# Kernel tuning notes

Hardware: AMD Instinct MI355X
Metric: run time of the kernel (lower is better)

The kernel has to match this reference:

```python
import jax, jax.numpy as jnp
import numpy as np

B = 65536
IN = 64
H = 16
PF = 64


def _linear_params(key, out_dim, in_dim):
    k1, k2 = jax.random.split(key)
    bound = 1.0 / np.sqrt(in_dim)
    W = jax.random.uniform(k1, (out_dim, in_dim), jnp.float32, -bound, bound)
    b = jax.random.uniform(k2, (out_dim,), jnp.float32, -bound, bound)
    return W, b


def setup_inputs() -> dict:
    key = jax.random.key(0)
    ks = jax.random.split(key, 20)
    inp = {}
    for i, name in enumerate(['a', 'v', 'l', 'p_a', 'p_v', 'p_l', 'mean']):
        inp[name] = jax.random.normal(ks[i], (B, IN), jnp.float32)
    inp['Wa'], inp['ba'] = _linear_params(ks[7], H, IN)
    inp['Wv'], inp['bv'] = _linear_params(ks[8], H, IN)
    inp['Wl'], inp['bl'] = _linear_params(ks[9], H, IN)
    inp['Wap'], inp['bap'] = _linear_params(ks[10], H, IN)
    inp['Wvp'], inp['bvp'] = _linear_params(ks[11], H, IN)
    inp['Wlp'], inp['blp'] = _linear_params(ks[12], H, IN)
    inp['Wf1'], inp['bf1'] = _linear_params(ks[13], PF, H ** 3 // 16)
    inp['Wfp1'], inp['bfp1'] = _linear_params(ks[14], PF, H ** 3 // 16)
    inp['Wng'], inp['bng'] = _linear_params(ks[15], 64, 128)
    inp['rm1'] = jnp.zeros((128,), jnp.float32)  # normGate2 running_mean buffers (eval mode)
    inp['rm2'] = jnp.zeros((128,), jnp.float32)
    return inp


def _maxpool2(x):
    # 2x2 stride-2 max pool over the last two dims of [B, Hd, Wd]
    b, hd, wd = x.shape
    return x.reshape(b, hd // 2, 2, wd // 2, 2).max(axis=(2, 4))


def _trimodal_fusion(x_h, y_h, z_h):
    # outer product [B,H,H] -> pool -> [B,H*H//4,1] bmm [B,1,H] -> pool -> flatten
    f = x_h[:, :, None] * y_h[:, None, :]            # [B,16,16]
    f = _maxpool2(f)                                 # [B,8,8]
    f = f.reshape(-1, H * H // 4, 1) * z_h[:, None, :]  # [B,64,16]
    f = _maxpool2(f)                                 # [B,32,8]
    return f.reshape(x_h.shape[0], -1)               # [B,256]


def _norm_gate(x, running_mean):
    # eval-mode normGate2: y = x * sigmoid(|x - running_mean|)
    return x * jax.nn.sigmoid(jnp.abs(x - running_mean))


def reference(a, v, l, p_a, p_v, p_l, mean,
              Wa, ba, Wv, bv, Wl, bl, Wap, bap, Wvp, bvp, Wlp, blp,
              Wf1, bf1, Wfp1, bfp1, Wng, bng, rm1, rm2):
    a_h = jax.nn.sigmoid(a @ Wa.T + ba)
    v_h = jax.nn.sigmoid(v @ Wv.T + bv)
    l_h = jax.nn.sigmoid(l @ Wl.T + bl)
    fusion_1 = jax.nn.leaky_relu(_trimodal_fusion(a_h, v_h, l_h) @ Wf1.T + bf1)

    pa_h = jax.nn.sigmoid(p_a @ Wap.T + bap)
    pv_h = jax.nn.sigmoid(p_v @ Wvp.T + bvp)
    pl_h = jax.nn.sigmoid(p_l @ Wlp.T + blp)
    fusion_2 = jax.nn.leaky_relu(_trimodal_fusion(pa_h, pv_h, pl_h) @ Wfp1.T + bfp1)

    out = _norm_gate(jnp.concatenate([fusion_2, mean], axis=1), rm1)   # [B,128]
    out = out @ Wng.T + bng                                            # [B,64]
    out = _norm_gate(jnp.concatenate([out, fusion_1], axis=1), rm2)    # [B,128]
    return out
```

## Files before the change

kernel.cpp:

```cpp
#include <hip/hip_runtime.h>
#include <hip/hip_bf16.h>


typedef __attribute__((ext_vector_type(8))) short short8;
typedef __attribute__((ext_vector_type(4))) float f32x4;

#define MFMA16(A, B, C) __builtin_amdgcn_mfma_f32_16x16x32_bf16((A), (B), (C), 0, 0, 0)

__device__ __forceinline__ float fast_sigmoid(float x) {
    return __builtin_amdgcn_rcpf(1.0f + __expf(-x));
}
__device__ __forceinline__ float gate(float x, float rm) {
    return x * fast_sigmoid(fabsf(x - rm));
}
__device__ __forceinline__ float lrelu(float x) {
    return x >= 0.0f ? x : 0.01f * x;
}
__device__ __forceinline__ short f2bf(float f) {
    union { float f; unsigned u; } x; x.f = f;
    unsigned r = (x.u + 0x7FFF + ((x.u >> 16) & 1)) >> 16;
    return (short)r;
}
__device__ __forceinline__ short8 pack8(const float* xs) {
    union { short8 s; __hip_bfloat162 h[4]; } u;
    #pragma unroll
    for (int i = 0; i < 4; ++i) {
        float2 t; t.x = xs[2 * i]; t.y = xs[2 * i + 1];
        u.h[i] = __float22bfloat162_rn(t);
    }
    return u.s;
}
__device__ __forceinline__ f32x4 pmax_xor(f32x4 v, int mask) {
    f32x4 r;
    #pragma unroll
    for (int i = 0; i < 4; ++i) r[i] = fmaxf(v[i], __shfl_xor(v[i], mask, 64));
    return r;
}

__device__ __forceinline__ void proj_mfma2r(const float4* in,
                                            const short8* __restrict__ wfr,
                                            const float* __restrict__ bias,
                                            int lane, f32x4& h0, f32x4& h1) {
    const int m = lane & 15;
    f32x4 a0; a0[0] = a0[1] = a0[2] = a0[3] = 0.0f;
    f32x4 a1 = a0;
    #pragma unroll
    for (int t = 0; t < 2; ++t) {
        const short8 frag = wfr[t * 64 + lane];
        float xs0[8] = {in[2*t].x, in[2*t].y, in[2*t].z, in[2*t].w,
                        in[2*t+1].x, in[2*t+1].y, in[2*t+1].z, in[2*t+1].w};
        float xs1[8] = {in[4+2*t].x, in[4+2*t].y, in[4+2*t].z, in[4+2*t].w,
                        in[4+2*t+1].x, in[4+2*t+1].y, in[4+2*t+1].z, in[4+2*t+1].w};
        a0 = MFMA16(pack8(xs0), frag, a0);
        a1 = MFMA16(pack8(xs1), frag, a1);
    }
    const float bn = bias[m];
    #pragma unroll
    for (int r = 0; r < 4; ++r) {
        h0[r] = fast_sigmoid(a0[r] + bn);
        h1[r] = fast_sigmoid(a1[r] + bn);
    }
}

__device__ __forceinline__ void stage_pools(f32x4 hx, f32x4 hy, f32x4 hz, int lane,
                                            float* __restrict__ sX,
                                            float* __restrict__ sY,
                                            float* __restrict__ sZ) {
    const int quad = lane >> 4, ln = lane & 15;
    f32x4 X = pmax_xor(hx, 1);
    f32x4 Y = pmax_xor(pmax_xor(hy, 1), 2);
    f32x4 Z = pmax_xor(hz, 1);
    #pragma unroll
    for (int r = 0; r < 4; ++r) {
        const int sm = quad * 4 + r;
        sX[(ln >> 1) * 16 + sm] = X[r];
        sY[(ln >> 2) * 16 + sm] = Y[r];
        sZ[(ln >> 1) * 16 + sm] = Z[r];
    }
}

__device__ __forceinline__ void fusion_mfma2(const short8* __restrict__ wfr,
                                             const float* __restrict__ bias,
                                             const float* __restrict__ sP0,
                                             const float* __restrict__ sP1,
                                             int lane,
                                             f32x4 acc0[4], f32x4 acc1[4]) {
    const int m = lane & 15, quad = lane >> 4;
    const float* sX0 = sP0; const float* sY0 = sP0 + 128; const float* sZ0 = sP0 + 192;
    const float* sX1 = sP1; const float* sY1 = sP1 + 128; const float* sZ1 = sP1 + 192;
    #pragma unroll
    for (int nt = 0; nt < 4; ++nt) {
        const float bb = bias[nt * 16 + m];
        acc0[nt][0] = acc0[nt][1] = acc0[nt][2] = acc0[nt][3] = bb;
        acc1[nt][0] = acc1[nt][1] = acc1[nt][2] = acc1[nt][3] = bb;
    }
    float zr0[8], zr1[8], xr0[8], xr1[8];
    #pragma unroll
    for (int j = 0; j < 8; ++j) {
        zr0[j] = sZ0[j * 16 + m]; zr1[j] = sZ1[j * 16 + m];
        xr0[j] = sX0[j * 16 + m]; xr1[j] = sX1[j * 16 + m];
    }
    const float yq0 = sY0[quad * 16 + m];
    const float yq1 = sY1[quad * 16 + m];
    #pragma unroll
    for (int t = 0; t < 8; ++t) {
        const float xy0 = xr0[t] * yq0;
        const float xy1 = xr1[t] * yq1;
        float p0[8], p1[8];
        #pragma unroll
        for (int j = 0; j < 8; ++j) { p0[j] = xy0 * zr0[j]; p1[j] = xy1 * zr1[j]; }
        const short8 af0 = pack8(p0);
        const short8 af1 = pack8(p1);
        #pragma unroll
        for (int nt = 0; nt < 4; ++nt) {
            const short8 frag = wfr[(t * 4 + nt) * 64 + lane];
            acc0[nt] = MFMA16(af0, frag, acc0[nt]);
            acc1[nt] = MFMA16(af1, frag, acc1[nt]);
        }
    }
}

__global__ __launch_bounds__(256, 2)
void fused_fwd(const float* __restrict__ a,  const float* __restrict__ v,
               const float* __restrict__ l,  const float* __restrict__ pa,
               const float* __restrict__ pv, const float* __restrict__ pl,
               const float* __restrict__ mean,
               const float* __restrict__ ba,  const float* __restrict__ bv_,
               const float* __restrict__ bl_, const float* __restrict__ bap,
               const float* __restrict__ bvp, const float* __restrict__ blp,
               const float* __restrict__ bf1, const float* __restrict__ bfp1,
               const float* __restrict__ bng,
               const float* __restrict__ rm1, const float* __restrict__ rm2,
               const short* __restrict__ ws, float* __restrict__ out) {
    __shared__ __align__(16) float sPool[4 * 2 * 320];
    __shared__ __align__(16) short sF2[2 * 2 * 1280];

    const int tid = threadIdx.x;
    const int lane = tid & 63;
    const int w = tid >> 6;
    const int m = lane & 15;
    const int quad = lane >> 4;
    const int wi = w & 1;
    const int srow0 = blockIdx.x * 64 + wi * 32;

    float* sP0 = sPool + w * 640;
    float* sP1 = sP0 + 320;

    const short8* projFr = (const short8*)ws;
    const short8* wfFr   = (const short8*)(ws + 6144);
    const short8* wfpFr  = (const short8*)(ws + 22528);
    const short8* wngFr  = (const short8*)(ws + 38912);

    if (w < 2) {
        float4 inA[8], inB[8], inC[8], inM[8];
        {
            const float* x0 = pa + (size_t)srow0 * 64;
            const float* x1 = pv + (size_t)srow0 * 64;
            const float* x2 = pl + (size_t)srow0 * 64;
            #pragma unroll
            for (int i = 0; i < 8; ++i) {
                const int tile = i >> 2, t = (i >> 1) & 1, hf = i & 1;
                const size_t off = (size_t)(tile * 16 + m) * 64 + t * 32 + quad * 8 + hf * 4;
                inA[i] = *(const float4*)(x0 + off);
                inB[i] = *(const float4*)(x1 + off);
                inC[i] = *(const float4*)(x2 + off);
                inM[i] = *(const float4*)(mean + (size_t)(srow0 + tile * 16 + m) * 64
                                          + t * 32 + quad * 8 + hf * 4);
            }
        }
        __builtin_amdgcn_sched_barrier(0);

        f32x4 hx0, hx1, hy0, hy1, hz0, hz1;
        proj_mfma2r(inA, projFr + 3 * 128, bap, lane, hx0, hx1);
        proj_mfma2r(inB, projFr + 4 * 128, bvp, lane, hy0, hy1);
        proj_mfma2r(inC, projFr + 5 * 128, blp, lane, hz0, hz1);
        stage_pools(hx0, hy0, hz0, lane, sP0, sP0 + 128, sP0 + 192);
        stage_pools(hx1, hy1, hz1, lane, sP1, sP1 + 128, sP1 + 192);

        f32x4 f20[4], f21[4];
        fusion_mfma2(wfpFr, bfp1, sP0, sP1, lane, f20, f21);

        short* sF0 = sF2 + wi * 2560;
        short* sF1 = sF0 + 1280;
        #pragma unroll
        for (int nt = 0; nt < 4; ++nt) {
            const float r1 = rm1[nt * 16 + m];
            #pragma unroll
            for (int r = 0; r < 4; ++r) {
                sF0[(quad * 4 + r) * 80 + nt * 16 + m] = f2bf(gate(lrelu(f20[nt][r]), r1));
                sF1[(quad * 4 + r) * 80 + nt * 16 + m] = f2bf(gate(lrelu(f21[nt][r]), r1));
            }
        }

        f32x4 h0[4], h1[4];
        #pragma unroll
        for (int nt = 0; nt < 4; ++nt) {
            const float bb = bng[nt * 16 + m];
            h0[nt][0] = h0[nt][1] = h0[nt][2] = h0[nt][3] = bb;
            h1[nt][0] = h1[nt][1] = h1[nt][2] = h1[nt][3] = bb;
        }
        #pragma unroll
        for (int t = 0; t < 2; ++t) {
            const short8 af0 = *(const short8*)(sF0 + m * 80 + t * 32 + quad * 8);
            const short8 af1 = *(const short8*)(sF1 + m * 80 + t * 32 + quad * 8);
            #pragma unroll
            for (int nt = 0; nt < 4; ++nt) {
                const short8 frag = wngFr[(t * 4 + nt) * 64 + lane];
                h0[nt] = MFMA16(af0, frag, h0[nt]);
                h1[nt] = MFMA16(af1, frag, h1[nt]);
            }
        }
        #pragma unroll
        for (int t2 = 0; t2 < 2; ++t2) {
            const float4* rp = (const float4*)(rm1 + 64 + t2 * 32 + quad * 8);
            float4 r0 = rp[0], r1 = rp[1];
            float4 u0 = inM[2 * t2], u1 = inM[2 * t2 + 1];
            float4 w0 = inM[4 + 2 * t2], w1 = inM[4 + 2 * t2 + 1];
            float g0[8] = { gate(u0.x, r0.x), gate(u0.y, r0.y), gate(u0.z, r0.z), gate(u0.w, r0.w),
                            gate(u1.x, r1.x), gate(u1.y, r1.y), gate(u1.z, r1.z), gate(u1.w, r1.w) };
            float g1[8] = { gate(w0.x, r0.x), gate(w0.y, r0.y), gate(w0.z, r0.z), gate(w0.w, r0.w),
                            gate(w1.x, r1.x), gate(w1.y, r1.y), gate(w1.z, r1.z), gate(w1.w, r1.w) };
            const short8 af0 = pack8(g0);
            const short8 af1 = pack8(g1);
            #pragma unroll
            for (int nt = 0; nt < 4; ++nt) {
                const short8 frag = wngFr[((2 + t2) * 4 + nt) * 64 + lane];
                h0[nt] = MFMA16(af0, frag, h0[nt]);
                h1[nt] = MFMA16(af1, frag, h1[nt]);
            }
        }

        #pragma unroll
        for (int nt = 0; nt < 4; ++nt) {
            const float r2a = rm2[nt * 16 + m];
            #pragma unroll
            for (int r = 0; r < 4; ++r) {
                const size_t row0 = (size_t)(srow0 + quad * 4 + r) * 128;
                const size_t row1 = (size_t)(srow0 + 16 + quad * 4 + r) * 128;
                out[row0 + nt * 16 + m] = gate(h0[nt][r], r2a);
                out[row1 + nt * 16 + m] = gate(h1[nt][r], r2a);
            }
        }
    } else {
        float4 inA[8], inB[8], inC[8];
        {
            const float* x0 = a + (size_t)srow0 * 64;
            const float* x1 = v + (size_t)srow0 * 64;
            const float* x2 = l + (size_t)srow0 * 64;
            #pragma unroll
            for (int i = 0; i < 8; ++i) {
                const int tile = i >> 2, t = (i >> 1) & 1, hf = i & 1;
                const size_t off = (size_t)(tile * 16 + m) * 64 + t * 32 + quad * 8 + hf * 4;
                inA[i] = *(const float4*)(x0 + off);
                inB[i] = *(const float4*)(x1 + off);
                inC[i] = *(const float4*)(x2 + off);
            }
        }
        __builtin_amdgcn_sched_barrier(0);

        f32x4 hx0, hx1, hy0, hy1, hz0, hz1;
        proj_mfma2r(inA, projFr + 0 * 128, ba, lane, hx0, hx1);
        proj_mfma2r(inB, projFr + 1 * 128, bv_, lane, hy0, hy1);
        proj_mfma2r(inC, projFr + 2 * 128, bl_, lane, hz0, hz1);
        stage_pools(hx0, hy0, hz0, lane, sP0, sP0 + 128, sP0 + 192);
        stage_pools(hx1, hy1, hz1, lane, sP1, sP1 + 128, sP1 + 192);

        f32x4 f10[4], f11[4];
        fusion_mfma2(wfFr, bf1, sP0, sP1, lane, f10, f11);

        #pragma unroll
        for (int nt = 0; nt < 4; ++nt) {
            const float r2b = rm2[64 + nt * 16 + m];
            #pragma unroll
            for (int r = 0; r < 4; ++r) {
                const size_t row0 = (size_t)(srow0 + quad * 4 + r) * 128;
                const size_t row1 = (size_t)(srow0 + 16 + quad * 4 + r) * 128;
                out[row0 + 64 + nt * 16 + m] = gate(lrelu(f10[nt][r]), r2b);
                out[row1 + 64 + nt * 16 + m] = gate(lrelu(f11[nt][r]), r2b);
            }
        }
    }
}

__global__ void build_frags(const float* __restrict__ Wa,  const float* __restrict__ Wv,
                            const float* __restrict__ Wl,  const float* __restrict__ Wap,
                            const float* __restrict__ Wvp, const float* __restrict__ Wlp,
                            const float* __restrict__ Wf1, const float* __restrict__ Wfp1,
                            const float* __restrict__ Wng, short* __restrict__ ws) {
    const int i = blockIdx.x * 256 + threadIdx.x;
    if (i >= 47104) return;
    float val;
    if (i < 6144) {
        const float* W[6] = {Wa, Wv, Wl, Wap, Wvp, Wlp};
        const int mi = i >> 10, r = i & 1023;
        const int t = r >> 9, lane = (r >> 3) & 63, j = r & 7;
        val = W[mi][(lane & 15) * 64 + t * 32 + (lane >> 4) * 8 + j];
    } else if (i < 38912) {
        int r = i - 6144;
        const float* W = (r < 16384) ? Wf1 : Wfp1;
        r &= 16383;
        const int tn = r >> 9, lane = (r >> 3) & 63, j = r & 7;
        const int t = tn >> 2, nt = tn & 3;
        val = W[(nt * 16 + (lane & 15)) * 256 + t * 32 + (lane >> 4) * 8 + j];
    } else {
        const int r = i - 38912;
        const int tn = r >> 9, lane = (r >> 3) & 63, j = r & 7;
        const int t = tn >> 2, nt = tn & 3;
        val = Wng[(nt * 16 + (lane & 15)) * 128 + t * 32 + (lane >> 4) * 8 + j];
    }
    ws[i] = f2bf(val);
}

extern "C" void kernel_launch(void* const* d_in, const int* in_sizes, int n_in,
                              void* d_out, int out_size, void* d_ws, size_t ws_size,
                              hipStream_t stream) {
    const float* a    = (const float*)d_in[0];
    const float* v    = (const float*)d_in[1];
    const float* l    = (const float*)d_in[2];
    const float* pa   = (const float*)d_in[3];
    const float* pv   = (const float*)d_in[4];
    const float* pl   = (const float*)d_in[5];
    const float* mean = (const float*)d_in[6];
    const float* Wa   = (const float*)d_in[7];
    const float* ba   = (const float*)d_in[8];
    const float* Wv   = (const float*)d_in[9];
    const float* bv   = (const float*)d_in[10];
    const float* Wl   = (const float*)d_in[11];
    const float* bl   = (const float*)d_in[12];
    const float* Wap  = (const float*)d_in[13];
    const float* bap  = (const float*)d_in[14];
    const float* Wvp  = (const float*)d_in[15];
    const float* bvp  = (const float*)d_in[16];
    const float* Wlp  = (const float*)d_in[17];
    const float* blp  = (const float*)d_in[18];
    const float* Wf1  = (const float*)d_in[19];
    const float* bf1  = (const float*)d_in[20];
    const float* Wfp1 = (const float*)d_in[21];
    const float* bfp1 = (const float*)d_in[22];
    const float* Wng  = (const float*)d_in[23];
    const float* bng  = (const float*)d_in[24];
    const float* rm1  = (const float*)d_in[25];
    const float* rm2  = (const float*)d_in[26];

    short* ws = (short*)d_ws;

    build_frags<<<184, 256, 0, stream>>>(Wa, Wv, Wl, Wap, Wvp, Wlp,
                                         Wf1, Wfp1, Wng, ws);
    fused_fwd<<<1024, 256, 0, stream>>>(a, v, l, pa, pv, pl, mean,
                                        ba, bv, bl, bap, bvp, blp,
                                        bf1, bfp1, bng, rm1, rm2,
                                        ws, (float*)d_out);
}
```

Measured before the change: 38.59 us.

## Stage weight fragments in LDS via async DMA and specialize blocks per branch

New measurement: 42.43 us. +9.9%, slower.

```diff
diff --git a/kernel.cpp b/kernel.cpp
--- a/kernel.cpp
+++ b/kernel.cpp
@@ -35,6 +35,13 @@
     #pragma unroll
     for (int i = 0; i < 4; ++i) r[i] = fmaxf(v[i], __shfl_xor(v[i], mask, 64));
     return r;
+}
+
+__device__ __forceinline__ void dma_1k(const short* src, short* dst_lds, int lane) {
+    __builtin_amdgcn_global_load_lds(
+        (const __attribute__((address_space(1))) unsigned int*)(const void*)(src + lane * 8),
+        (__attribute__((address_space(3))) unsigned int*)(void*)(dst_lds),
+        16, 0, 0);
 }
 
 __device__ __forceinline__ void proj_mfma2r(const float4* in,
@@ -132,151 +139,164 @@
                const float* __restrict__ bng,
                const float* __restrict__ rm1, const float* __restrict__ rm2,
                const short* __restrict__ ws, float* __restrict__ out) {
-    __shared__ __align__(16) float sPool[4 * 2 * 320];
-    __shared__ __align__(16) short sF2[2 * 2 * 1280];
+    __shared__ __align__(16) short sFrag[27648];
+    __shared__ __align__(16) float sScr[4][1280];
 
     const int tid = threadIdx.x;
     const int lane = tid & 63;
     const int w = tid >> 6;
     const int m = lane & 15;
     const int quad = lane >> 4;
-    const int wi = w & 1;
-    const int srow0 = blockIdx.x * 64 + wi * 32;
-
-    float* sP0 = sPool + w * 640;
+    const int p1 = blockIdx.x & 1;
+    const int p  = blockIdx.x >> 1;
+
+    {
+        const int nU = p1 ? 38 : 54;
+        for (int u = w; u < nU; u += 4) {
+            const short* src;
+            if (u < 6)       src = ws + (p1 ? 0 : 3072) + u * 512;
+            else if (u < 38) src = ws + (p1 ? 6144 : 22528) + (u - 6) * 512;
+            else             src = ws + 38912 + (u - 38) * 512;
+            dma_1k(src, sFrag + u * 512, lane);
+        }
+    }
+    __syncthreads();
+
+    const short8* projT = (const short8*)sFrag;
+    const short8* fusT  = (const short8*)(sFrag + 3072);
+    const short8* ngT   = (const short8*)(sFrag + 19456);
+
+    float* sP0 = sScr[w];
     float* sP1 = sP0 + 320;
-
-    const short8* projFr = (const short8*)ws;
-    const short8* wfFr   = (const short8*)(ws + 6144);
-    const short8* wfpFr  = (const short8*)(ws + 22528);
-    const short8* wngFr  = (const short8*)(ws + 38912);
-
-    if (w < 2) {
-        float4 inA[8], inB[8], inC[8], inM[8];
-        {
-            const float* x0 = pa + (size_t)srow0 * 64;
-            const float* x1 = pv + (size_t)srow0 * 64;
-            const float* x2 = pl + (size_t)srow0 * 64;
-            #pragma unroll
-            for (int i = 0; i < 8; ++i) {
-                const int tile = i >> 2, t = (i >> 1) & 1, hf = i & 1;
-                const size_t off = (size_t)(tile * 16 + m) * 64 + t * 32 + quad * 8 + hf * 4;
-                inA[i] = *(const float4*)(x0 + off);
-                inB[i] = *(const float4*)(x1 + off);
-                inC[i] = *(const float4*)(x2 + off);
-                inM[i] = *(const float4*)(mean + (size_t)(srow0 + tile * 16 + m) * 64
-                                          + t * 32 + quad * 8 + hf * 4);
-            }
-        }
-        __builtin_amdgcn_sched_barrier(0);
-
-        f32x4 hx0, hx1, hy0, hy1, hz0, hz1;
-        proj_mfma2r(inA, projFr + 3 * 128, bap, lane, hx0, hx1);
-        proj_mfma2r(inB, projFr + 4 * 128, bvp, lane, hy0, hy1);
-        proj_mfma2r(inC, projFr + 5 * 128, blp, lane, hz0, hz1);
-        stage_pools(hx0, hy0, hz0, lane, sP0, sP0 + 128, sP0 + 192);
-        stage_pools(hx1, hy1, hz1, lane, sP1, sP1 + 128, sP1 + 192);
-
-        f32x4 f20[4], f21[4];
-        fusion_mfma2(wfpFr, bfp1, sP0, sP1, lane, f20, f21);
-
-        short* sF0 = sF2 + wi * 2560;
-        short* sF1 = sF0 + 1280;
-        #pragma unroll
-        for (int nt = 0; nt < 4; ++nt) {
-            const float r1 = rm1[nt * 16 + m];
-            #pragma unroll
-            for (int r = 0; r < 4; ++r) {
-                sF0[(quad * 4 + r) * 80 + nt * 16 + m] = f2bf(gate(lrelu(f20[nt][r]), r1));
-                sF1[(quad * 4 + r) * 80 + nt * 16 + m] = f2bf(gate(lrelu(f21[nt][r]), r1));
-            }
-        }
-
-        f32x4 h0[4], h1[4];
-        #pragma unroll
-        for (int nt = 0; nt < 4; ++nt) {
-            const float bb = bng[nt * 16 + m];
-            h0[nt][0] = h0[nt][1] = h0[nt][2] = h0[nt][3] = bb;
-            h1[nt][0] = h1[nt][1] = h1[nt][2] = h1[nt][3] = bb;
-        }
-        #pragma unroll
-        for (int t = 0; t < 2; ++t) {
-            const short8 af0 = *(const short8*)(sF0 + m * 80 + t * 32 + quad * 8);
-            const short8 af1 = *(const short8*)(sF1 + m * 80 + t * 32 + quad * 8);
+    short* sF0 = (short*)sScr[w];
+    short* sF1 = sF0 + 1280;
+
+    for (int c = 0; c < 2; ++c) {
+        const int srow0 = (p * 2 + c) * 128 + w * 32;
+
+        if (!p1) {
+            float4 inA[8], inB[8], inC[8], inM[8];
+            {
+                const float* x0 = pa + (size_t)srow0 * 64;
+                const float* x1 = pv + (size_t)srow0 * 64;
+                const float* x2 = pl + (size_t)srow0 * 64;
+                #pragma unroll
+                for (int i = 0; i < 8; ++i) {
+                    const int tile = i >> 2, t = (i >> 1) & 1, hf = i & 1;
+                    const size_t off = (size_t)(tile * 16 + m) * 64 + t * 32 + quad * 8 + hf * 4;
+                    inA[i] = *(const float4*)(x0 + off);
+                    inB[i] = *(const float4*)(x1 + off);
+                    inC[i] = *(const float4*)(x2 + off);
+                    inM[i] = *(const float4*)(mean + (size_t)(srow0 + tile * 16 + m) * 64
+                                              + t * 32 + quad * 8 + hf * 4);
+                }
+            }
+
+            f32x4 hx0, hx1, hy0, hy1, hz0, hz1;
+            proj_mfma2r(inA, projT + 0 * 128, bap, lane, hx0, hx1);
+            proj_mfma2r(inB, projT + 1 * 128, bvp, lane, hy0, hy1);
+            proj_mfma2r(inC, projT + 2 * 128, blp, lane, hz0, hz1);
+            stage_pools(hx0, hy0, hz0, lane, sP0, sP0 + 128, sP0 + 192);
+            stage_pools(hx1, hy1, hz1, lane, sP1, sP1 + 128, sP1 + 192);
+
+            f32x4 f20[4], f21[4];
+            fusion_mfma2(fusT, bfp1, sP0, sP1, lane, f20, f21);
+
             #pragma unroll
             for (int nt = 0; nt < 4; ++nt) {
-                const short8 frag = wngFr[(t * 4 + nt) * 64 + lane];
-                h0[nt] = MFMA16(af0, frag, h0[nt]);
-                h1[nt] = MFMA16(af1, frag, h1[nt]);
-            }
-        }
-        #pragma unroll
-        for (int t2 = 0; t2 < 2; ++t2) {
-            const float4* rp = (const float4*)(rm1 + 64 + t2 * 32 + quad * 8);
-            float4 r0 = rp[0], r1 = rp[1];
-            float4 u0 = inM[2 * t2], u1 = inM[2 * t2 + 1];
-            float4 w0 = inM[4 + 2 * t2], w1 = inM[4 + 2 * t2 + 1];
-            float g0[8] = { gate(u0.x, r0.x), gate(u0.y, r0.y), gate(u0.z, r0.z), gate(u0.w, r0.w),
-                            gate(u1.x, r1.x), gate(u1.y, r1.y), gate(u1.z, r1.z), gate(u1.w, r1.w) };
-            float g1[8] = { gate(w0.x, r0.x), gate(w0.y, r0.y), gate(w0.z, r0.z), gate(w0.w, r0.w),
-                            gate(w1.x, r1.x), gate(w1.y, r1.y), gate(w1.z, r1.z), gate(w1.w, r1.w) };
-            const short8 af0 = pack8(g0);
-            const short8 af1 = pack8(g1);
+                const float r1 = rm1[nt * 16 + m];
+                #pragma unroll
+                for (int r = 0; r < 4; ++r) {
+                    sF0[(quad * 4 + r) * 80 + nt * 16 + m] = f2bf(gate(lrelu(f20[nt][r]), r1));
+                    sF1[(quad * 4 + r) * 80 + nt * 16 + m] = f2bf(gate(lrelu(f21[nt][r]), r1));
+                }
+            }
+
+            f32x4 h0[4], h1[4];
             #pragma unroll
             for (int nt = 0; nt < 4; ++nt) {
-                const short8 frag = wngFr[((2 + t2) * 4 + nt) * 64 + lane];
-                h0[nt] = MFMA16(af0, frag, h0[nt]);
-                h1[nt] = MFMA16(af1, frag, h1[nt]);
-            }
-        }
-
-        #pragma unroll
-        for (int nt = 0; nt < 4; ++nt) {
-            const float r2a = rm2[nt * 16 + m];
-            #pragma unroll
-            for (int r = 0; r < 4; ++r) {
-                const size_t row0 = (size_t)(srow0 + quad * 4 + r) * 128;
-                const size_t row1 = (size_t)(srow0 + 16 + quad * 4 + r) * 128;
-                out[row0 + nt * 16 + m] = gate(h0[nt][r], r2a);
-                out[row1 + nt * 16 + m] = gate(h1[nt][r], r2a);
-            }
-        }
-    } else {
-        float4 inA[8], inB[8], inC[8];
-        {
-            const float* x0 = a + (size_t)srow0 * 64;
-            const float* x1 = v + (size_t)srow0 * 64;
-            const float* x2 = l + (size_t)srow0 * 64;
-            #pragma unroll
-            for (int i = 0; i < 8; ++i) {
-                const int tile = i >> 2, t = (i >> 1) & 1, hf = i & 1;
-                const size_t off = (size_t)(tile * 16 + m) * 64 + t * 32 + quad * 8 + hf * 4;
-                inA[i] = *(const float4*)(x0 + off);
-                inB[i] = *(const float4*)(x1 + off);
-                inC[i] = *(const float4*)(x2 + off);
-            }
-        }
-        __builtin_amdgcn_sched_barrier(0);
-
-        f32x4 hx0, hx1, hy0, hy1, hz0, hz1;
-        proj_mfma2r(inA, projFr + 0 * 128, ba, lane, hx0, hx1);
-        proj_mfma2r(inB, projFr + 1 * 128, bv_, lane, hy0, hy1);
-        proj_mfma2r(inC, projFr + 2 * 128, bl_, lane, hz0, hz1);
-        stage_pools(hx0, hy0, hz0, lane, sP0, sP0 + 128, sP0 + 192);
-        stage_pools(hx1, hy1, hz1, lane, sP1, sP1 + 128, sP1 + 192);
-
-        f32x4 f10[4], f11[4];
-        fusion_mfma2(wfFr, bf1, sP0, sP1, lane, f10, f11);
-
-        #pragma unroll
-        for (int nt = 0; nt < 4; ++nt) {
-            const float r2b = rm2[64 + nt * 16 + m];
-            #pragma unroll
-            for (int r = 0; r < 4; ++r) {
-                const size_t row0 = (size_t)(srow0 + quad * 4 + r) * 128;
-                const size_t row1 = (size_t)(srow0 + 16 + quad * 4 + r) * 128;
-                out[row0 + 64 + nt * 16 + m] = gate(lrelu(f10[nt][r]), r2b);
-                out[row1 + 64 + nt * 16 + m] = gate(lrelu(f11[nt][r]), r2b);
+                const float bb = bng[nt * 16 + m];
+                h0[nt][0] = h0[nt][1] = h0[nt][2] = h0[nt][3] = bb;
+                h1[nt][0] = h1[nt][1] = h1[nt][2] = h1[nt][3] = bb;
+            }
+            #pragma unroll
+            for (int t = 0; t < 2; ++t) {
+                const short8 af0 = *(const short8*)(sF0 + m * 80 + t * 32 + quad * 8);
+                const short8 af1 = *(const short8*)(sF1 + m * 80 + t * 32 + quad * 8);
+                #pragma unroll
+                for (int nt = 0; nt < 4; ++nt) {
+                    const short8 frag = ngT[(t * 4 + nt) * 64 + lane];
+                    h0[nt] = MFMA16(af0, frag, h0[nt]);
+                    h1[nt] = MFMA16(af1, frag, h1[nt]);
+                }
+            }
+            #pragma unroll
+            for (int t2 = 0; t2 < 2; ++t2) {
+                const float4* rp = (const float4*)(rm1 + 64 + t2 * 32 + quad * 8);
+                float4 r0 = rp[0], r1 = rp[1];
+                float4 u0 = inM[2 * t2], u1 = inM[2 * t2 + 1];
+                float4 w0 = inM[4 + 2 * t2], w1 = inM[4 + 2 * t2 + 1];
+                float g0[8] = { gate(u0.x, r0.x), gate(u0.y, r0.y), gate(u0.z, r0.z), gate(u0.w, r0.w),
+                                gate(u1.x, r1.x), gate(u1.y, r1.y), gate(u1.z, r1.z), gate(u1.w, r1.w) };
+                float g1[8] = { gate(w0.x, r0.x), gate(w0.y, r0.y), gate(w0.z, r0.z), gate(w0.w, r0.w),
+                                gate(w1.x, r1.x), gate(w1.y, r1.y), gate(w1.z, r1.z), gate(w1.w, r1.w) };
+                const short8 af0 = pack8(g0);
+                const short8 af1 = pack8(g1);
+                #pragma unroll
+                for (int nt = 0; nt < 4; ++nt) {
+                    const short8 frag = ngT[((2 + t2) * 4 + nt) * 64 + lane];
+                    h0[nt] = MFMA16(af0, frag, h0[nt]);
+                    h1[nt] = MFMA16(af1, frag, h1[nt]);
+                }
+            }
+
+            #pragma unroll
+            for (int nt = 0; nt < 4; ++nt) {
+                const float r2a = rm2[nt * 16 + m];
+                #pragma unroll
+                for (int r = 0; r < 4; ++r) {
+                    const size_t row0 = (size_t)(srow0 + quad * 4 + r) * 128;
+                    const size_t row1 = (size_t)(srow0 + 16 + quad * 4 + r) * 128;
+                    out[row0 + nt * 16 + m] = gate(h0[nt][r], r2a);
+                    out[row1 + nt * 16 + m] = gate(h1[nt][r], r2a);
+                }
+            }
+        } else {
+            float4 inA[8], inB[8], inC[8];
+            {
+                const float* x0 = a + (size_t)srow0 * 64;
+                const float* x1 = v + (size_t)srow0 * 64;
+                const float* x2 = l + (size_t)srow0 * 64;
+                #pragma unroll
+                for (int i = 0; i < 8; ++i) {
+                    const int tile = i >> 2, t = (i >> 1) & 1, hf = i & 1;
+                    const size_t off = (size_t)(tile * 16 + m) * 64 + t * 32 + quad * 8 + hf * 4;
+                    inA[i] = *(const float4*)(x0 + off);
+                    inB[i] = *(const float4*)(x1 + off);
+                    inC[i] = *(const float4*)(x2 + off);
+                }
+            }
+
+            f32x4 hx0, hx1, hy0, hy1, hz0, hz1;
+            proj_mfma2r(inA, projT + 0 * 128, ba, lane, hx0, hx1);
+            proj_mfma2r(inB, projT + 1 * 128, bv_, lane, hy0, hy1);
+            proj_mfma2r(inC, projT + 2 * 128, bl_, lane, hz0, hz1);
+            stage_pools(hx0, hy0, hz0, lane, sP0, sP0 + 128, sP0 + 192);
+            stage_pools(hx1, hy1, hz1, lane, sP1, sP1 + 128, sP1 + 192);
+
+            f32x4 f10[4], f11[4];
+            fusion_mfma2(fusT, bf1, sP0, sP1, lane, f10, f11);
+
+            #pragma unroll
+            for (int nt = 0; nt < 4; ++nt) {
+                const float r2b = rm2[64 + nt * 16 + m];
+                #pragma unroll
+                for (int r = 0; r < 4; ++r) {
+                    const size_t row0 = (size_t)(srow0 + quad * 4 + r) * 128;
+                    const size_t row1 = (size_t)(srow0 + 16 + quad * 4 + r) * 128;
+                    out[row0 + 64 + nt * 16 + m] = gate(lrelu(f10[nt][r]), r2b);
+                    out[row1 + 64 + nt * 16 + m] = gate(lrelu(f11[nt][r]), r2b);
+                }
             }
         }
     }
@@ -346,8 +366,8 @@
 
     build_frags<<<184, 256, 0, stream>>>(Wa, Wv, Wl, Wap, Wvp, Wlp,
                                          Wf1, Wfp1, Wng, ws);
-    fused_fwd<<<1024, 256, 0, stream>>>(a, v, l, pa, pv, pl, mean,
-                                        ba, bv, bl, bap, bvp, blp,
-                                        bf1, bfp1, bng, rm1, rm2,
-                                        ws, (float*)d_out);
-}
+    fused_fwd<<<512, 256, 0, stream>>>(a, v, l, pa, pv, pl, mean,
+                                       ba, bv, bl, bap, bvp, blp,
+                                       bf1, bfp1, bng, rm1, rm2,
+                                       ws, (float*)d_out);
+}
```
